# Kernel optimization log

Measured on AMD Instinct MI355X. Metric: run time of the kernel, lower is better.

The kernel has to match this reference:

```python
import jax, jax.numpy as jnp
import numpy as np
from jax import lax

B, T, H = 32768, 64, 16
VOCAB_USER = 600001
VOCAB_LAUNCH = 3


def setup_inputs() -> dict:
    key = jax.random.key(0)
    ks = jax.random.split(key, 10)
    s = 1.0 / np.sqrt(H)
    return {
        "user_id": jax.random.randint(ks[0], (B,), 0, VOCAB_USER),
        "launch_seq": jax.random.randint(ks[1], (B, T), 0, VOCAB_LAUNCH),
        "user_emb": jax.random.normal(ks[2], (VOCAB_USER, H), dtype=jnp.float32),
        "launch_emb": jax.random.normal(ks[3], (VOCAB_LAUNCH, H), dtype=jnp.float32),
        "W_ih": jax.random.uniform(ks[4], (3 * H, H), jnp.float32, -s, s),
        "W_hh": jax.random.uniform(ks[5], (3 * H, H), jnp.float32, -s, s),
        "b_ih": jax.random.uniform(ks[6], (3 * H,), jnp.float32, -s, s),
        "b_hh": jax.random.uniform(ks[7], (3 * H,), jnp.float32, -s, s),
        "fc_W": jax.random.uniform(ks[8], (1, 2 * H), jnp.float32, -s, s),
        "fc_b": jax.random.uniform(ks[9], (1,), jnp.float32, -s, s),
    }


def reference(user_id, launch_seq, user_emb, launch_emb, W_ih, W_hh, b_ih, b_hh, fc_W, fc_b):
    u = user_emb[user_id]                      # (B, H)
    x = launch_emb[launch_seq]                 # (B, T, H)
    # precompute input contributions to the gates for all timesteps
    gx_all = jnp.einsum('bth,gh->btg', x, W_ih) + b_ih  # (B, T, 3H)

    def step(h, gx):
        gh = h @ W_hh.T + b_hh                 # (B, 3H)
        r = jax.nn.sigmoid(gx[:, :H] + gh[:, :H])
        z = jax.nn.sigmoid(gx[:, H:2 * H] + gh[:, H:2 * H])
        n = jnp.tanh(gx[:, 2 * H:] + r * gh[:, 2 * H:])
        h_new = (1.0 - z) * n + z * h
        return h_new, h_new

    h0 = jnp.zeros((x.shape[0], H), dtype=x.dtype)
    _, hs = lax.scan(step, h0, jnp.swapaxes(gx_all, 0, 1))  # hs: (T, B, H)
    pooled = jnp.mean(hs, axis=0)              # (B, H)
    fc_in = jnp.concatenate([u, pooled], axis=1)  # (B, 2H)
    return fc_in @ fc_W.T + fc_b               # (B, 1)
```

## Files before the change

kernel.cpp:

```cpp
#include <hip/hip_runtime.h>


#define NB 32768
#define TT 64

static __device__ __forceinline__ float fast_exp2(float x) { return __builtin_amdgcn_exp2f(x); }
static __device__ __forceinline__ float fast_rcp(float x)  { return __builtin_amdgcn_rcpf(x); }

__global__ __launch_bounds__(64) void gru_kernel(
    const int* __restrict__ user_id,
    const int* __restrict__ launch_seq,
    const float* __restrict__ user_emb,
    const float* __restrict__ launch_emb,
    const float* __restrict__ W_ih,
    const float* __restrict__ W_hh,
    const float* __restrict__ b_ih,
    const float* __restrict__ b_hh,
    const float* __restrict__ fc_W,
    const float* __restrict__ fc_b,
    float* __restrict__ out)
{
    constexpr float L  = 1.4426950408889634f;
    constexpr float L2 = 2.8853900817779268f;

    __shared__ float4 gx4[3 * 16];
    __shared__ int    seq_lds[4 * 64];
    __shared__ float4 hbuf[2][16];

    const int tid = threadIdx.x;
    const int e   = tid & 15;
    const int j   = tid >> 4;
    const long long sampBase = (long long)blockIdx.x * 4;

    for (int idx = tid; idx < 144; idx += 64) {
        int s = idx / 48;
        int g = idx - s * 48;
        float dot = b_ih[g];
        #pragma unroll
        for (int k = 0; k < 16; ++k)
            dot = fmaf(W_ih[g * 16 + k], launch_emb[s * 16 + k], dot);
        int ge = g & 15;
        float* dst = (float*)&gx4[s * 16 + ge];
        if (g < 16)       dst[0] = -L * (dot + b_hh[g]);
        else if (g < 32)  dst[1] = -L * (dot + b_hh[g]);
        else              dst[2] =  L2 * dot;
    }

    ((int4*)seq_lds)[tid] = ((const int4*)(launch_seq + sampBase * TT))[tid];

    float Wr[16], Wz[16], Wn[16];
    #pragma unroll
    for (int k = 0; k < 16; ++k) {
        Wr[k] = -L * W_hh[e * 16 + k];
        Wz[k] = -L * W_hh[(16 + e) * 16 + k];
        Wn[k] =  L2 * W_hh[(32 + e) * 16 + k];
    }
    const float bhn = L2 * b_hh[32 + e];

    ((float*)hbuf[0])[tid] = 0.0f;
    float h = 0.0f, pool = 0.0f;
    __syncthreads();

    auto step = [&](const float4* __restrict__ hin, float* __restrict__ hout, int t) {
        int s = seq_lds[j * 64 + t];
        float4 g4 = gx4[s * 16 + e];
        float4 a0 = hin[j * 4 + 0];
        float4 a1 = hin[j * 4 + 1];
        float4 a2 = hin[j * 4 + 2];
        float4 a3 = hin[j * 4 + 3];
        float hv[16] = {a0.x, a0.y, a0.z, a0.w, a1.x, a1.y, a1.z, a1.w,
                        a2.x, a2.y, a2.z, a2.w, a3.x, a3.y, a3.z, a3.w};
        float ar = g4.x, az = g4.y, an = bhn;
        #pragma unroll
        for (int k = 0; k < 16; ++k) {
            ar = fmaf(Wr[k], hv[k], ar);
            az = fmaf(Wz[k], hv[k], az);
            an = fmaf(Wn[k], hv[k], an);
        }
        float r = fast_rcp(1.0f + fast_exp2(ar));
        float z = fast_rcp(1.0f + fast_exp2(az));
        float y = fmaf(r, an, g4.z);
        float q = fast_rcp(1.0f + fast_exp2(y));
        float n = fmaf(-2.0f, q, 1.0f);
        h = fmaf(z, h - n, n);
        pool += h;
        hout[j * 16 + e] = h;
    };

    for (int t = 0; t < TT; t += 2) {
        step(hbuf[0], (float*)hbuf[1], t);
        __syncthreads();
        step(hbuf[1], (float*)hbuf[0], t + 1);
        __syncthreads();
    }

    pool *= (1.0f / 64.0f);
    int uid = user_id[sampBase + j];
    float u = user_emb[(long long)uid * 16 + e];
    float val = fc_W[e] * u + fc_W[16 + e] * pool;
    val += __shfl_xor(val, 8, 16);
    val += __shfl_xor(val, 4, 16);
    val += __shfl_xor(val, 2, 16);
    val += __shfl_xor(val, 1, 16);
    if (e == 0) out[sampBase + j] = val + fc_b[0];
}

extern "C" void kernel_launch(void* const* d_in, const int* in_sizes, int n_in,
                              void* d_out, int out_size, void* d_ws, size_t ws_size,
                              hipStream_t stream) {
    const int*   user_id    = (const int*)d_in[0];
    const int*   launch_seq = (const int*)d_in[1];
    const float* user_emb   = (const float*)d_in[2];
    const float* launch_emb = (const float*)d_in[3];
    const float* W_ih       = (const float*)d_in[4];
    const float* W_hh       = (const float*)d_in[5];
    const float* b_ih       = (const float*)d_in[6];
    const float* b_hh       = (const float*)d_in[7];
    const float* fc_W       = (const float*)d_in[8];
    const float* fc_b       = (const float*)d_in[9];
    float* out = (float*)d_out;

    gru_kernel<<<dim3(NB / 4), dim3(64), 0, stream>>>(
        user_id, launch_seq, user_emb, launch_emb,
        W_ih, W_hh, b_ih, b_hh, fc_W, fc_b, out);
}
```

Baseline: 155.0 us.

## Compute GRU recurrent matmul with split-bf16 MFMA over 16 samples per wave

Each 64-thread block now handles 16 samples. The per-step hidden-to-gate matmul runs on 16x16x32 bf16 MFMA instructions, with fp32 precision approximated by hi/lo bf16 splitting (three MFMAs per gate). Hidden state is exchanged through swizzled LDS buffers, and sequence indices are packed to bytes. The goal is to replace the scalar FMA chains, cut the number of blocks, and amortise per-step syncs across more samples. The cost is extra conversion work, MFMA latency on the serial recurrence path, and slightly reduced precision from the bf16 split.

```diff
diff --git a/kernel.cpp b/kernel.cpp
--- a/kernel.cpp
+++ b/kernel.cpp
@@ -1,13 +1,25 @@
 #include <hip/hip_runtime.h>
+#include <hip/hip_bf16.h>
+#include <string.h>
 
 
-#define NB 32768
-#define TT 64
+#define NBLK 2048
 
-static __device__ __forceinline__ float fast_exp2(float x) { return __builtin_amdgcn_exp2f(x); }
-static __device__ __forceinline__ float fast_rcp(float x)  { return __builtin_amdgcn_rcpf(x); }
+typedef __attribute__((ext_vector_type(8))) short short8;
+typedef __attribute__((ext_vector_type(4))) float floatx4;
 
-__global__ __launch_bounds__(64) void gru_kernel(
+static __device__ __forceinline__ float fexp2(float x) { return __builtin_amdgcn_exp2f(x); }
+static __device__ __forceinline__ float frcp(float x)  { return __builtin_amdgcn_rcpf(x); }
+
+static __device__ __forceinline__ unsigned short bf16_bits(float f) {
+    __hip_bfloat16 b = __float2bfloat16(f);
+    union { __hip_bfloat16 b; unsigned short u; } cv; cv.b = b; return cv.u;
+}
+static __device__ __forceinline__ float bf16_f32(unsigned short u) {
+    unsigned v = ((unsigned)u) << 16; float f; memcpy(&f, &v, 4); return f;
+}
+
+__global__ __launch_bounds__(64) void gru_mfma(
     const int* __restrict__ user_id,
     const int* __restrict__ launch_seq,
     const float* __restrict__ user_emb,
@@ -23,14 +35,27 @@
     constexpr float L  = 1.4426950408889634f;
     constexpr float L2 = 2.8853900817779268f;
 
-    __shared__ float4 gx4[3 * 16];
-    __shared__ int    seq_lds[4 * 64];
-    __shared__ float4 hbuf[2][16];
+    __shared__ float gxr[48], gxz[48], gxn[48];
+    __shared__ unsigned char  seqb[16 * 68];
+    __shared__ unsigned short hhi[16 * 32];
+    __shared__ unsigned short hlo[16 * 32];
 
-    const int tid = threadIdx.x;
-    const int e   = tid & 15;
-    const int j   = tid >> 4;
-    const long long sampBase = (long long)blockIdx.x * 4;
+    const int tid  = threadIdx.x;
+    const int col  = tid & 15;
+    const int quad = tid >> 4;
+    const long long sampBase = (long long)blockIdx.x * 16;
+
+    {
+        int r = tid >> 2, w = tid & 3;
+        const int* sp = launch_seq + (sampBase + r) * 64 + w * 16;
+        #pragma unroll
+        for (int g = 0; g < 4; ++g) {
+            int4 v = ((const int4*)sp)[g];
+            unsigned pk = (unsigned)v.x | ((unsigned)v.y << 8) |
+                          ((unsigned)v.z << 16) | ((unsigned)v.w << 24);
+            *(unsigned*)(seqb + r * 68 + w * 16 + g * 4) = pk;
+        }
+    }
 
     for (int idx = tid; idx < 144; idx += 64) {
         int s = idx / 48;
@@ -39,70 +64,112 @@
         #pragma unroll
         for (int k = 0; k < 16; ++k)
             dot = fmaf(W_ih[g * 16 + k], launch_emb[s * 16 + k], dot);
-        int ge = g & 15;
-        float* dst = (float*)&gx4[s * 16 + ge];
-        if (g < 16)       dst[0] = -L * (dot + b_hh[g]);
-        else if (g < 32)  dst[1] = -L * (dot + b_hh[g]);
-        else              dst[2] =  L2 * dot;
+        int d = g & 15;
+        if (g < 16)      gxr[s * 16 + d] = -L * (dot + b_hh[g]);
+        else if (g < 32) gxz[s * 16 + d] = -L * (dot + b_hh[g]);
+        else             gxn[s * 16 + d] =  L2 * dot;
     }
 
-    ((int4*)seq_lds)[tid] = ((const int4*)(launch_seq + sampBase * TT))[tid];
+    for (int i = tid; i < 256; i += 64) {
+        ((unsigned*)hhi)[i] = 0u;
+        ((unsigned*)hlo)[i] = 0u;
+    }
 
-    float Wr[16], Wz[16], Wn[16];
+    short8 Brh, Brl, Bzh, Bzl, Bnh, Bnl;
     #pragma unroll
-    for (int k = 0; k < 16; ++k) {
-        Wr[k] = -L * W_hh[e * 16 + k];
-        Wz[k] = -L * W_hh[(16 + e) * 16 + k];
-        Wn[k] =  L2 * W_hh[(32 + e) * 16 + k];
+    for (int j = 0; j < 8; ++j) {
+        int k = quad * 8 + j;
+        float wr = 0.f, wz = 0.f, wn = 0.f;
+        if (k < 16) {
+            wr = -L  * W_hh[(col)      * 16 + k];
+            wz = -L  * W_hh[(16 + col) * 16 + k];
+            wn =  L2 * W_hh[(32 + col) * 16 + k];
+        }
+        unsigned short h;
+        h = bf16_bits(wr); Brh[j] = (short)h; Brl[j] = (short)bf16_bits(wr - bf16_f32(h));
+        h = bf16_bits(wz); Bzh[j] = (short)h; Bzl[j] = (short)bf16_bits(wz - bf16_f32(h));
+        h = bf16_bits(wn); Bnh[j] = (short)h; Bnl[j] = (short)bf16_bits(wn - bf16_f32(h));
     }
-    const float bhn = L2 * b_hh[32 + e];
 
-    ((float*)hbuf[0])[tid] = 0.0f;
-    float h = 0.0f, pool = 0.0f;
+    const float bhn = L2 * b_hh[32 + col];
+    const floatx4 Cn_init = {bhn, bhn, bhn, bhn};
+
+    const int a_off = col * 64 + (((quad + col + (col >> 2)) & 3) << 4);
+    int w_off[4], seq_base[4];
+    #pragma unroll
+    for (int i = 0; i < 4; ++i) {
+        int s = quad * 4 + i;
+        w_off[i] = s * 64 + ((((col >> 3) + s + (s >> 2)) & 3) << 4) + (col & 7) * 2;
+        seq_base[i] = s * 68;
+    }
+
+    floatx4 h    = {0.f, 0.f, 0.f, 0.f};
+    floatx4 pool = {0.f, 0.f, 0.f, 0.f};
+    short8 Ahi = {0, 0, 0, 0, 0, 0, 0, 0};
+    short8 Alo = {0, 0, 0, 0, 0, 0, 0, 0};
+
     __syncthreads();
 
-    auto step = [&](const float4* __restrict__ hin, float* __restrict__ hout, int t) {
-        int s = seq_lds[j * 64 + t];
-        float4 g4 = gx4[s * 16 + e];
-        float4 a0 = hin[j * 4 + 0];
-        float4 a1 = hin[j * 4 + 1];
-        float4 a2 = hin[j * 4 + 2];
-        float4 a3 = hin[j * 4 + 3];
-        float hv[16] = {a0.x, a0.y, a0.z, a0.w, a1.x, a1.y, a1.z, a1.w,
-                        a2.x, a2.y, a2.z, a2.w, a3.x, a3.y, a3.z, a3.w};
-        float ar = g4.x, az = g4.y, an = bhn;
+    #pragma unroll 4
+    for (int t = 0; t < 64; ++t) {
+        int s0 = seqb[seq_base[0] + t];
+        int s1 = seqb[seq_base[1] + t];
+        int s2 = seqb[seq_base[2] + t];
+        int s3 = seqb[seq_base[3] + t];
+
+        floatx4 accr, accz;
+        accr.x = gxr[(s0 << 4) + col]; accr.y = gxr[(s1 << 4) + col];
+        accr.z = gxr[(s2 << 4) + col]; accr.w = gxr[(s3 << 4) + col];
+        accz.x = gxz[(s0 << 4) + col]; accz.y = gxz[(s1 << 4) + col];
+        accz.z = gxz[(s2 << 4) + col]; accz.w = gxz[(s3 << 4) + col];
+        float gn[4];
+        gn[0] = gxn[(s0 << 4) + col]; gn[1] = gxn[(s1 << 4) + col];
+        gn[2] = gxn[(s2 << 4) + col]; gn[3] = gxn[(s3 << 4) + col];
+
+        accr = __builtin_amdgcn_mfma_f32_16x16x32_bf16(Ahi, Brh, accr, 0, 0, 0);
+        accr = __builtin_amdgcn_mfma_f32_16x16x32_bf16(Alo, Brh, accr, 0, 0, 0);
+        accr = __builtin_amdgcn_mfma_f32_16x16x32_bf16(Ahi, Brl, accr, 0, 0, 0);
+        accz = __builtin_amdgcn_mfma_f32_16x16x32_bf16(Ahi, Bzh, accz, 0, 0, 0);
+        accz = __builtin_amdgcn_mfma_f32_16x16x32_bf16(Alo, Bzh, accz, 0, 0, 0);
+        accz = __builtin_amdgcn_mfma_f32_16x16x32_bf16(Ahi, Bzl, accz, 0, 0, 0);
+        floatx4 accn;
+        accn = __builtin_amdgcn_mfma_f32_16x16x32_bf16(Ahi, Bnh, Cn_init, 0, 0, 0);
+        accn = __builtin_amdgcn_mfma_f32_16x16x32_bf16(Alo, Bnh, accn, 0, 0, 0);
+        accn = __builtin_amdgcn_mfma_f32_16x16x32_bf16(Ahi, Bnl, accn, 0, 0, 0);
+
         #pragma unroll
-        for (int k = 0; k < 16; ++k) {
-            ar = fmaf(Wr[k], hv[k], ar);
-            az = fmaf(Wz[k], hv[k], az);
-            an = fmaf(Wn[k], hv[k], an);
+        for (int i = 0; i < 4; ++i) {
+            float r  = frcp(1.0f + fexp2(accr[i]));
+            float z  = frcp(1.0f + fexp2(accz[i]));
+            float y  = fmaf(r, accn[i], gn[i]);
+            float n  = fmaf(-2.0f, frcp(1.0f + fexp2(y)), 1.0f);
+            float hn = fmaf(z, h[i] - n, n);
+            h[i] = hn;
+            pool[i] += hn;
+            unsigned short hb = bf16_bits(hn);
+            *(unsigned short*)((char*)hhi + w_off[i]) = hb;
+            *(unsigned short*)((char*)hlo + w_off[i]) = bf16_bits(hn - bf16_f32(hb));
         }
-        float r = fast_rcp(1.0f + fast_exp2(ar));
-        float z = fast_rcp(1.0f + fast_exp2(az));
-        float y = fmaf(r, an, g4.z);
-        float q = fast_rcp(1.0f + fast_exp2(y));
-        float n = fmaf(-2.0f, q, 1.0f);
-        h = fmaf(z, h - n, n);
-        pool += h;
-        hout[j * 16 + e] = h;
-    };
 
-    for (int t = 0; t < TT; t += 2) {
-        step(hbuf[0], (float*)hbuf[1], t);
         __syncthreads();
-        step(hbuf[1], (float*)hbuf[0], t + 1);
-        __syncthreads();
+        Ahi = *(const short8*)((const char*)hhi + a_off);
+        Alo = *(const short8*)((const char*)hlo + a_off);
     }
 
-    pool *= (1.0f / 64.0f);
-    int uid = user_id[sampBase + j];
-    float u = user_emb[(long long)uid * 16 + e];
-    float val = fc_W[e] * u + fc_W[16 + e] * pool;
-    val += __shfl_xor(val, 8, 16);
-    val += __shfl_xor(val, 4, 16);
-    val += __shfl_xor(val, 2, 16);
-    val += __shfl_xor(val, 1, 16);
-    if (e == 0) out[sampBase + j] = val + fc_b[0];
+    const float fw1 = fc_W[col];
+    const float fw2 = fc_W[16 + col] * (1.0f / 64.0f);
+    #pragma unroll
+    for (int i = 0; i < 4; ++i) {
+        int s = quad * 4 + i;
+        int uid = user_id[sampBase + s];
+        float u = user_emb[(long long)uid * 16 + col];
+        float v = fmaf(u, fw1, pool[i] * fw2);
+        v += __shfl_xor(v, 1);
+        v += __shfl_xor(v, 2);
+        v += __shfl_xor(v, 4);
+        v += __shfl_xor(v, 8);
+        if (col == 0) out[sampBase + s] = v + fc_b[0];
+    }
 }
 
 extern "C" void kernel_launch(void* const* d_in, const int* in_sizes, int n_in,
@@ -120,7 +187,7 @@
     const float* fc_b       = (const float*)d_in[9];
     float* out = (float*)d_out;
 
-    gru_kernel<<<dim3(NB / 4), dim3(64), 0, stream>>>(
+    gru_mfma<<<dim3(NBLK), dim3(64), 0, stream>>>(
         user_id, launch_seq, user_emb, launch_emb,
         W_ih, W_hh, b_ih, b_hh, fc_W, fc_b, out);
 }
```

Measured after the change: 145.6 us. -6.1%, faster.
